# Performance work log

Measured on AMD Instinct MI355X. Metric: run time of the kernel, lower is better.

## Reference

```python
import jax, jax.numpy as jnp
import numpy as np

N = 100000
E = 3200000
IN_C = 500
HID = 256
OUT_C = 64
K = 10


def setup_inputs() -> dict:
    key = jax.random.key(0)
    k1, k2, k3, k4, k5 = jax.random.split(key, 5)
    node_feat = jax.random.normal(k1, (N, IN_C), dtype=jnp.float32)
    edge_index = jax.random.randint(k2, (2, E), 0, N, dtype=jnp.int64)
    # learned params (torch nn.Linear: y = x @ W.T + b)
    s1 = 1.0 / np.sqrt(IN_C)
    W1 = jax.random.uniform(k3, (HID, IN_C), jnp.float32, -s1, s1)
    b1 = jnp.zeros((HID,), jnp.float32)
    s2 = 1.0 / np.sqrt(HID)
    W2 = jax.random.uniform(k4, (OUT_C, HID), jnp.float32, -s2, s2)
    b2 = jnp.zeros((OUT_C,), jnp.float32)
    s3 = 1.0 / np.sqrt(OUT_C)
    proj_w = jax.random.uniform(k5, (OUT_C,), jnp.float32, -s3, s3)
    proj_b = jnp.zeros((), jnp.float32)
    return {"node_feat": node_feat, "edge_index": edge_index,
            "W1": W1, "b1": b1, "W2": W2, "b2": b2,
            "proj_w": proj_w, "proj_b": proj_b}


def reference(node_feat, edge_index, W1, b1, W2, b2, proj_w, proj_b):
    # MLP part (dropout p=0.0 / eval -> identity)
    x = jax.nn.relu(node_feat @ W1.T + b1)      # [N, HID]
    x = x @ W2.T + b2                            # [N, OUT_C]

    # gcn_norm with add_remaining_self_loops(fill=1):
    # existing self loops are dropped and replaced by unit-weight loops; with
    # all-ones edge_weight this equals zero-weighting self-loop edges and
    # appending N unit-weight self loops (static shapes, same math).
    row, col = edge_index[0], edge_index[1]
    loop = jnp.arange(N, dtype=edge_index.dtype)
    w = (row != col).astype(x.dtype)             # [E]
    full_row = jnp.concatenate([row, loop])      # [E+N]
    full_col = jnp.concatenate([col, loop])
    full_w = jnp.concatenate([w, jnp.ones((N,), x.dtype)])
    deg = jax.ops.segment_sum(full_w, full_col, num_segments=N)
    dinv = jnp.where(deg > 0, deg ** -0.5, 0.0).astype(x.dtype)
    norm = dinv[full_row] * full_w * dinv[full_col]  # [E+N]

    # K-hop propagation: gather -> scale -> scatter-add
    preds = [x]
    for _ in range(K):
        msg = norm[:, None] * x[full_row]        # [E+N, OUT_C]
        x = jax.ops.segment_sum(msg, full_col, num_segments=N)
        preds.append(x)
    pps = jnp.stack(preds, axis=1)               # [N, K+1, OUT_C]

    # sigmoid attention combine: proj = Linear(OUT_C, 1)
    score = jax.nn.sigmoid(jnp.einsum('nkc,c->nk', pps, proj_w) + proj_b)
    out = jnp.einsum('nk,nkc->nc', score, pps)   # [N, OUT_C]
    return out
```

## Files before the change

### kernel.cpp

```cpp
#include <hip/hip_runtime.h>
#include <math.h>

#define NN 100000
#define EE 3200000
#define INC 500
#define HIDN 256
#define OC 64
#define KHOP 10

typedef __attribute__((ext_vector_type(4))) float f4;
typedef __attribute__((ext_vector_type(4))) unsigned short us4;
typedef __attribute__((ext_vector_type(8))) unsigned short us8;

__device__ __forceinline__ float bf2f(unsigned short u) {
    return __uint_as_float(((unsigned int)u) << 16);
}
__device__ __forceinline__ unsigned short f2bf(float f) {
    unsigned int i = __float_as_uint(f);
    i += 0x7fffu + ((i >> 16) & 1u);
    return (unsigned short)(i >> 16);
}

__global__ __launch_bounds__(256) void gemm1_k(
    const float* __restrict__ feat, const float* __restrict__ W1,
    const float* __restrict__ b1, unsigned short* __restrict__ h)
{
    __shared__ float sA[16][64];
    __shared__ float sB[16][256];
    const int t  = threadIdx.x;
    const int m0 = blockIdx.x * 64;
    const int tx = t & 31;
    const int ty = t >> 5;
    float acc[8][8];
#pragma unroll
    for (int i = 0; i < 8; ++i)
#pragma unroll
        for (int j = 0; j < 8; ++j) acc[i][j] = 0.f;

    const int sm  = t >> 2;
    const int skq = (t & 3) * 4;

    for (int k0 = 0; k0 < INC; k0 += 16) {
        {
            int m = m0 + sm;
            f4 v = {0.f, 0.f, 0.f, 0.f};
            if (m < NN) {
                if (k0 + skq + 3 < INC) {
                    v = *reinterpret_cast<const f4*>(&feat[(size_t)m * INC + k0 + skq]);
                } else {
#pragma unroll
                    for (int i = 0; i < 4; ++i) {
                        int k = k0 + skq + i;
                        if (k < INC) v[i] = feat[(size_t)m * INC + k];
                    }
                }
            }
#pragma unroll
            for (int i = 0; i < 4; ++i) sA[skq + i][sm] = v[i];
        }
#pragma unroll
        for (int p = 0; p < 4; ++p) {
            int j = sm + p * 64;
            f4 v = {0.f, 0.f, 0.f, 0.f};
            if (k0 + skq + 3 < INC) {
                v = *reinterpret_cast<const f4*>(&W1[(size_t)j * INC + k0 + skq]);
            } else {
#pragma unroll
                for (int i = 0; i < 4; ++i) {
                    int k = k0 + skq + i;
                    if (k < INC) v[i] = W1[(size_t)j * INC + k];
                }
            }
#pragma unroll
            for (int i = 0; i < 4; ++i) sB[skq + i][j] = v[i];
        }
        __syncthreads();
#pragma unroll
        for (int k = 0; k < 16; ++k) {
            f4 a0 = *reinterpret_cast<const f4*>(&sA[k][ty * 8]);
            f4 a1 = *reinterpret_cast<const f4*>(&sA[k][ty * 8 + 4]);
            f4 c0 = *reinterpret_cast<const f4*>(&sB[k][tx * 4]);
            f4 c1 = *reinterpret_cast<const f4*>(&sB[k][128 + tx * 4]);
            float a[8] = {a0[0], a0[1], a0[2], a0[3], a1[0], a1[1], a1[2], a1[3]};
            float b[8] = {c0[0], c0[1], c0[2], c0[3], c1[0], c1[1], c1[2], c1[3]};
#pragma unroll
            for (int i = 0; i < 8; ++i)
#pragma unroll
                for (int j = 0; j < 8; ++j) acc[i][j] += a[i] * b[j];
        }
        __syncthreads();
    }
#pragma unroll
    for (int i = 0; i < 8; ++i) {
        int m = m0 + ty * 8 + i;
        if (m >= NN) continue;
        us4 o0, o1;
#pragma unroll
        for (int j = 0; j < 4; ++j) {
            float v0 = acc[i][j] + b1[tx * 4 + j];
            o0[j] = f2bf(v0 > 0.f ? v0 : 0.f);
            float v1 = acc[i][j + 4] + b1[128 + tx * 4 + j];
            o1[j] = f2bf(v1 > 0.f ? v1 : 0.f);
        }
        *reinterpret_cast<us4*>(&h[(size_t)m * HIDN + tx * 4]) = o0;
        *reinterpret_cast<us4*>(&h[(size_t)m * HIDN + 128 + tx * 4]) = o1;
    }
}

__global__ __launch_bounds__(256) void gemm2_k(
    const unsigned short* __restrict__ h, const float* __restrict__ W2,
    const float* __restrict__ b2, const float* __restrict__ pw,
    const float* __restrict__ pbp, float* __restrict__ out,
    unsigned short* __restrict__ xb)
{
    __shared__ unsigned short sA[32][64];
    __shared__ float sB[32][64];
    __shared__ float sX[64][65];
    const int t  = threadIdx.x;
    const int m0 = blockIdx.x * 64;
    const int tx = t & 15;
    const int ty = t >> 4;
    float acc[4][4];
#pragma unroll
    for (int i = 0; i < 4; ++i)
#pragma unroll
        for (int j = 0; j < 4; ++j) acc[i][j] = 0.f;

    const int am  = t >> 2;
    const int akq = (t & 3) * 8;

    for (int k0 = 0; k0 < HIDN; k0 += 32) {
        {
            int m = m0 + am;
            us8 v;
#pragma unroll
            for (int i = 0; i < 8; ++i) v[i] = 0;
            if (m < NN)
                v = *reinterpret_cast<const us8*>(&h[(size_t)m * HIDN + k0 + akq]);
#pragma unroll
            for (int i = 0; i < 8; ++i) sA[akq + i][am] = v[i];
        }
#pragma unroll
        for (int p = 0; p < 2; ++p) {
            int fid = t + p * 256;
            int c   = fid >> 3;
            int kq  = (fid & 7) * 4;
            f4 v = *reinterpret_cast<const f4*>(&W2[(size_t)c * HIDN + k0 + kq]);
#pragma unroll
            for (int i = 0; i < 4; ++i) sB[kq + i][c] = v[i];
        }
        __syncthreads();
#pragma unroll
        for (int k = 0; k < 32; ++k) {
            us4 av = *reinterpret_cast<const us4*>(&sA[k][ty * 4]);
            f4  bv = *reinterpret_cast<const f4*>(&sB[k][tx * 4]);
            float a[4] = {bf2f(av[0]), bf2f(av[1]), bf2f(av[2]), bf2f(av[3])};
#pragma unroll
            for (int i = 0; i < 4; ++i)
#pragma unroll
                for (int j = 0; j < 4; ++j) acc[i][j] += a[i] * bv[j];
        }
        __syncthreads();
    }
#pragma unroll
    for (int i = 0; i < 4; ++i)
#pragma unroll
        for (int j = 0; j < 4; ++j)
            sX[ty * 4 + i][tx * 4 + j] = acc[i][j] + b2[tx * 4 + j];
    __syncthreads();
    const int row  = t >> 2;
    const int part = t & 3;
    float v = 0.f;
#pragma unroll
    for (int i = 0; i < 16; ++i) {
        int c = part * 16 + i;
        v += sX[row][c] * pw[c];
    }
    v += __shfl_xor(v, 1);
    v += __shfl_xor(v, 2);
    float s = 1.f / (1.f + expf(-(v + pbp[0])));
    int m = m0 + row;
    if (m < NN) {
#pragma unroll
        for (int i = 0; i < 16; ++i) {
            int c = part * 16 + i;
            float val = sX[row][c];
            out[(size_t)m * OC + c] = s * val;
            xb[(size_t)m * OC + c]  = f2bf(val);
        }
    }
}

__global__ void deg_k(const int* __restrict__ ei, int* __restrict__ cnt) {
    int e = blockIdx.x * blockDim.x + threadIdx.x;
    if (e >= EE) return;
    int r = ei[e], c = ei[EE + e];
    if (r != c) atomicAdd(&cnt[c], 1);
}

__global__ __launch_bounds__(256) void scan1_k(const int* __restrict__ cnt,
                                               int* __restrict__ tmp,
                                               int* __restrict__ bsum) {
    __shared__ int sd[256];
    int t = threadIdx.x;
    int i = blockIdx.x * 256 + t;
    int v = (i < NN) ? cnt[i] : 0;
    int x = v;
    sd[t] = x;
    __syncthreads();
    for (int off = 1; off < 256; off <<= 1) {
        int y = (t >= off) ? sd[t - off] : 0;
        __syncthreads();
        x += y;
        sd[t] = x;
        __syncthreads();
    }
    if (i < NN) tmp[i] = x;
    if (t == 255) bsum[blockIdx.x] = x;
}

__global__ __launch_bounds__(512) void scan2_k(const int* __restrict__ bsum,
                                               int* __restrict__ boff, int nb) {
    __shared__ int sd[512];
    int t = threadIdx.x;
    int v = (t < nb) ? bsum[t] : 0;
    int x = v;
    sd[t] = x;
    __syncthreads();
    for (int off = 1; off < 512; off <<= 1) {
        int y = (t >= off) ? sd[t - off] : 0;
        __syncthreads();
        x += y;
        sd[t] = x;
        __syncthreads();
    }
    boff[t] = x - v;
}

__global__ __launch_bounds__(256) void scan3_k(const int* __restrict__ cnt,
                                               const int* __restrict__ tmp,
                                               const int* __restrict__ boff,
                                               int* __restrict__ rowptr) {
    int i = blockIdx.x * 256 + threadIdx.x;
    if (i < NN) {
        rowptr[i] = boff[blockIdx.x] + tmp[i] - cnt[i];
        if (i == NN - 1) rowptr[NN] = boff[blockIdx.x] + tmp[i];
    }
}

__global__ void dinv_k(const int* __restrict__ cnt, float* __restrict__ dinv) {
    int i = blockIdx.x * blockDim.x + threadIdx.x;
    if (i < NN) dinv[i] = rsqrtf((float)cnt[i] + 1.0f);
}

__global__ void fill_k(const int* __restrict__ ei, const int* __restrict__ rowptr,
                       int* __restrict__ fpos, const float* __restrict__ dinv,
                       int* __restrict__ csrc, float* __restrict__ cnrm) {
    int e = blockIdx.x * blockDim.x + threadIdx.x;
    if (e >= EE) return;
    int r = ei[e], c = ei[EE + e];
    if (r != c) {
        int p = rowptr[c] + atomicAdd(&fpos[c], 1);
        csrc[p] = r;
        cnrm[p] = dinv[r] * dinv[c];
    }
}

__global__ __launch_bounds__(256) void prop_k(
    const unsigned short* __restrict__ xin, unsigned short* __restrict__ xout,
    const int* __restrict__ rowptr, const int* __restrict__ csrc,
    const float* __restrict__ cnrm, const float* __restrict__ dinv,
    const float* __restrict__ pw, const float* __restrict__ pbp,
    float* __restrict__ out)
{
    int wid  = blockIdx.x * 4 + (threadIdx.x >> 6);
    int lane = threadIdx.x & 63;
    if (wid >= NN) return;
    float di = dinv[wid];
    float a0 = di * di * bf2f(xin[(size_t)wid * OC + lane]);
    float a1 = 0.f, a2 = 0.f, a3 = 0.f;
    int p0 = rowptr[wid], p1 = rowptr[wid + 1];
    for (int base = p0; base < p1; base += 64) {
        int n = p1 - base;
        if (n > 64) n = 64;
        int   sv = 0;
        float wv = 0.f;
        if (lane < n) {
            sv = csrc[base + lane];
            wv = cnrm[base + lane];
        }
        int j = 0;
        for (; j + 4 <= n; j += 4) {
            int   r0 = __shfl(sv, j    );
            int   r1 = __shfl(sv, j + 1);
            int   r2 = __shfl(sv, j + 2);
            int   r3 = __shfl(sv, j + 3);
            float w0 = __shfl(wv, j    );
            float w1 = __shfl(wv, j + 1);
            float w2 = __shfl(wv, j + 2);
            float w3 = __shfl(wv, j + 3);
            float x0 = bf2f(xin[(size_t)r0 * OC + lane]);
            float x1 = bf2f(xin[(size_t)r1 * OC + lane]);
            float x2 = bf2f(xin[(size_t)r2 * OC + lane]);
            float x3 = bf2f(xin[(size_t)r3 * OC + lane]);
            a0 += w0 * x0;
            a1 += w1 * x1;
            a2 += w2 * x2;
            a3 += w3 * x3;
        }
        for (; j < n; ++j) {
            int   r  = __shfl(sv, j);
            float wj = __shfl(wv, j);
            a0 += wj * bf2f(xin[(size_t)r * OC + lane]);
        }
    }
    float acc = (a0 + a1) + (a2 + a3);
    xout[(size_t)wid * OC + lane] = f2bf(acc);
    float v = acc * pw[lane];
#pragma unroll
    for (int off = 32; off > 0; off >>= 1) v += __shfl_xor(v, off);
    float s = 1.f / (1.f + expf(-(v + pbp[0])));
    out[(size_t)wid * OC + lane] += s * acc;
}

extern "C" void kernel_launch(void* const* d_in, const int* in_sizes, int n_in,
                              void* d_out, int out_size, void* d_ws, size_t ws_size,
                              hipStream_t stream)
{
    (void)in_sizes; (void)n_in; (void)out_size; (void)ws_size;
    const float* feat = (const float*)d_in[0];
    const int*   ei   = (const int*)d_in[1];
    const float* W1   = (const float*)d_in[2];
    const float* b1   = (const float*)d_in[3];
    const float* W2   = (const float*)d_in[4];
    const float* b2   = (const float*)d_in[5];
    const float* pw   = (const float*)d_in[6];
    const float* pbp  = (const float*)d_in[7];
    float* out = (float*)d_out;

    char* w = (char*)d_ws;
    auto carve = [&](size_t bytes) {
        char* p = w;
        w += (bytes + 255) & ~(size_t)255;
        return p;
    };
    unsigned short* h    = (unsigned short*)carve((size_t)NN * HIDN * 2);
    unsigned short* xb0  = (unsigned short*)carve((size_t)NN * OC * 2);
    unsigned short* xb1  = (unsigned short*)carve((size_t)NN * OC * 2);
    int*   csrc   = (int*)carve((size_t)EE * 4);
    float* cnrm   = (float*)carve((size_t)EE * 4);
    int*   cnt    = (int*)carve((size_t)NN * 4);
    int*   tmp    = (int*)carve((size_t)NN * 4);
    int*   bsum   = (int*)carve(4096);
    int*   boff   = (int*)carve(4096);
    int*   rowptr = (int*)carve((size_t)(NN + 1) * 4);
    int*   fpos   = (int*)carve((size_t)NN * 4);
    float* dinv   = (float*)carve((size_t)NN * 4);

    hipMemsetAsync(cnt, 0, (size_t)NN * 4, stream);
    hipMemsetAsync(fpos, 0, (size_t)NN * 4, stream);

    gemm1_k<<<1563, 256, 0, stream>>>(feat, W1, b1, h);
    deg_k<<<12500, 256, 0, stream>>>(ei, cnt);
    scan1_k<<<391, 256, 0, stream>>>(cnt, tmp, bsum);
    scan2_k<<<1, 512, 0, stream>>>(bsum, boff, 391);
    scan3_k<<<391, 256, 0, stream>>>(cnt, tmp, boff, rowptr);
    dinv_k<<<391, 256, 0, stream>>>(cnt, dinv);
    fill_k<<<12500, 256, 0, stream>>>(ei, rowptr, fpos, dinv, csrc, cnrm);
    gemm2_k<<<1563, 256, 0, stream>>>(h, W2, b2, pw, pbp, out, xb0);

    unsigned short* xi = xb0;
    unsigned short* xo = xb1;
    for (int k = 0; k < KHOP; ++k) {
        prop_k<<<25000, 256, 0, stream>>>(xi, xo, rowptr, csrc, cnrm, dinv, pw, pbp, out);
        unsigned short* t2 = xi; xi = xo; xo = t2;
    }
}
```

Measured before the change: 1.777 ms.

## Use bf16 MFMA for first GEMM, pack edge arrays, defer attention combine

The first GEMM moves from scalar FP32 FMA to bf16 MFMA 16x16x32 instructions. Operands are converted to bf16 when staged into padded shared memory, and K is zero-padded to 512. Edge source index and norm are packed into one int2 array so each propagation loop needs a single load. When the workspace is large enough, every hop's features are kept and one combine kernel computes the sigmoid-weighted sum, instead of a read-modify-write of the fp32 output after each hop. Converting the GEMM inputs to bf16 reduces precision.

```diff
diff --git a/kernel.cpp b/kernel.cpp
--- a/kernel.cpp
+++ b/kernel.cpp
@@ -7,10 +7,13 @@
 #define HIDN 256
 #define OC 64
 #define KHOP 10
+#define LDA 40
 
 typedef __attribute__((ext_vector_type(4))) float f4;
 typedef __attribute__((ext_vector_type(4))) unsigned short us4;
 typedef __attribute__((ext_vector_type(8))) unsigned short us8;
+typedef __attribute__((ext_vector_type(8))) short short8;
+typedef __attribute__((ext_vector_type(4))) float f32x4;
 
 __device__ __forceinline__ float bf2f(unsigned short u) {
     return __uint_as_float(((unsigned int)u) << 16);
@@ -20,90 +23,96 @@
     i += 0x7fffu + ((i >> 16) & 1u);
     return (unsigned short)(i >> 16);
 }
+__device__ __forceinline__ us8 pack8(f4 a, f4 b) {
+    us8 r;
+    r[0] = f2bf(a[0]); r[1] = f2bf(a[1]); r[2] = f2bf(a[2]); r[3] = f2bf(a[3]);
+    r[4] = f2bf(b[0]); r[5] = f2bf(b[1]); r[6] = f2bf(b[2]); r[7] = f2bf(b[3]);
+    return r;
+}
 
 __global__ __launch_bounds__(256) void gemm1_k(
     const float* __restrict__ feat, const float* __restrict__ W1,
     const float* __restrict__ b1, unsigned short* __restrict__ h)
 {
-    __shared__ float sA[16][64];
-    __shared__ float sB[16][256];
-    const int t  = threadIdx.x;
-    const int m0 = blockIdx.x * 64;
-    const int tx = t & 31;
-    const int ty = t >> 5;
-    float acc[8][8];
-#pragma unroll
-    for (int i = 0; i < 8; ++i)
-#pragma unroll
-        for (int j = 0; j < 8; ++j) acc[i][j] = 0.f;
-
-    const int sm  = t >> 2;
-    const int skq = (t & 3) * 4;
-
-    for (int k0 = 0; k0 < INC; k0 += 16) {
+    __shared__ unsigned short sA[64 * LDA];
+    __shared__ unsigned short sB[256 * LDA];
+
+    const int t    = threadIdx.x;
+    const int m0   = blockIdx.x * 64;
+    const int wc   = t >> 6;
+    const int lane = t & 63;
+    const int lg   = lane >> 4;
+    const int lm   = lane & 15;
+
+    f32x4 acc[4][4];
+#pragma unroll
+    for (int i = 0; i < 4; ++i)
+#pragma unroll
+        for (int j = 0; j < 4; ++j) acc[i][j] = (f32x4){0.f, 0.f, 0.f, 0.f};
+
+    const int arow = t >> 2;
+    const int akq  = (t & 3) * 8;
+
+    for (int k0 = 0; k0 < 512; k0 += 32) {
         {
-            int m = m0 + sm;
-            f4 v = {0.f, 0.f, 0.f, 0.f};
-            if (m < NN) {
-                if (k0 + skq + 3 < INC) {
-                    v = *reinterpret_cast<const f4*>(&feat[(size_t)m * INC + k0 + skq]);
-                } else {
-#pragma unroll
-                    for (int i = 0; i < 4; ++i) {
-                        int k = k0 + skq + i;
-                        if (k < INC) v[i] = feat[(size_t)m * INC + k];
-                    }
-                }
+            int gm = m0 + arow;
+            int kk = k0 + akq;
+            f4 va = {0.f, 0.f, 0.f, 0.f}, vb = {0.f, 0.f, 0.f, 0.f};
+            if (gm < NN) {
+                const float* p = &feat[(size_t)gm * INC + kk];
+                if (kk     < INC) va = *reinterpret_cast<const f4*>(p);
+                if (kk + 4 < INC) vb = *reinterpret_cast<const f4*>(p + 4);
             }
-#pragma unroll
-            for (int i = 0; i < 4; ++i) sA[skq + i][sm] = v[i];
-        }
-#pragma unroll
-        for (int p = 0; p < 4; ++p) {
-            int j = sm + p * 64;
-            f4 v = {0.f, 0.f, 0.f, 0.f};
-            if (k0 + skq + 3 < INC) {
-                v = *reinterpret_cast<const f4*>(&W1[(size_t)j * INC + k0 + skq]);
-            } else {
-#pragma unroll
-                for (int i = 0; i < 4; ++i) {
-                    int k = k0 + skq + i;
-                    if (k < INC) v[i] = W1[(size_t)j * INC + k];
-                }
+            *reinterpret_cast<us8*>(&sA[arow * LDA + akq]) = pack8(va, vb);
+        }
+#pragma unroll
+        for (int p = 0; p < 2; ++p) {
+            int fid = t + p * 256;
+            int row = fid >> 1;
+            int kq  = (fid & 1) * 16;
+            int kk  = k0 + kq;
+            const float* pp = &W1[(size_t)row * INC + kk];
+            f4 v0 = {0.f,0.f,0.f,0.f}, v1 = {0.f,0.f,0.f,0.f};
+            f4 v2 = {0.f,0.f,0.f,0.f}, v3 = {0.f,0.f,0.f,0.f};
+            if (kk      < INC) v0 = *reinterpret_cast<const f4*>(pp);
+            if (kk + 4  < INC) v1 = *reinterpret_cast<const f4*>(pp + 4);
+            if (kk + 8  < INC) v2 = *reinterpret_cast<const f4*>(pp + 8);
+            if (kk + 12 < INC) v3 = *reinterpret_cast<const f4*>(pp + 12);
+            *reinterpret_cast<us8*>(&sB[row * LDA + kq])     = pack8(v0, v1);
+            *reinterpret_cast<us8*>(&sB[row * LDA + kq + 8]) = pack8(v2, v3);
+        }
+        __syncthreads();
+        short8 aF[4], bF[4];
+#pragma unroll
+        for (int mi = 0; mi < 4; ++mi)
+            aF[mi] = *reinterpret_cast<const short8*>(&sA[(mi * 16 + lm) * LDA + lg * 8]);
+#pragma unroll
+        for (int ni = 0; ni < 4; ++ni)
+            bF[ni] = *reinterpret_cast<const short8*>(&sB[(wc * 64 + ni * 16 + lm) * LDA + lg * 8]);
+#pragma unroll
+        for (int mi = 0; mi < 4; ++mi)
+#pragma unroll
+            for (int ni = 0; ni < 4; ++ni)
+                acc[mi][ni] = __builtin_amdgcn_mfma_f32_16x16x32_bf16(
+                    aF[mi], bF[ni], acc[mi][ni], 0, 0, 0);
+        __syncthreads();
+    }
+    float bias[4];
+#pragma unroll
+    for (int ni = 0; ni < 4; ++ni) bias[ni] = b1[wc * 64 + ni * 16 + lm];
+#pragma unroll
+    for (int mi = 0; mi < 4; ++mi) {
+#pragma unroll
+        for (int r = 0; r < 4; ++r) {
+            int row = m0 + mi * 16 + lg * 4 + r;
+            if (row >= NN) continue;
+            size_t base = (size_t)row * HIDN + wc * 64;
+#pragma unroll
+            for (int ni = 0; ni < 4; ++ni) {
+                float v = acc[mi][ni][r] + bias[ni];
+                h[base + ni * 16 + lm] = f2bf(v > 0.f ? v : 0.f);
             }
-#pragma unroll
-            for (int i = 0; i < 4; ++i) sB[skq + i][j] = v[i];
-        }
-        __syncthreads();
-#pragma unroll
-        for (int k = 0; k < 16; ++k) {
-            f4 a0 = *reinterpret_cast<const f4*>(&sA[k][ty * 8]);
-            f4 a1 = *reinterpret_cast<const f4*>(&sA[k][ty * 8 + 4]);
-            f4 c0 = *reinterpret_cast<const f4*>(&sB[k][tx * 4]);
-            f4 c1 = *reinterpret_cast<const f4*>(&sB[k][128 + tx * 4]);
-            float a[8] = {a0[0], a0[1], a0[2], a0[3], a1[0], a1[1], a1[2], a1[3]};
-            float b[8] = {c0[0], c0[1], c0[2], c0[3], c1[0], c1[1], c1[2], c1[3]};
-#pragma unroll
-            for (int i = 0; i < 8; ++i)
-#pragma unroll
-                for (int j = 0; j < 8; ++j) acc[i][j] += a[i] * b[j];
-        }
-        __syncthreads();
-    }
-#pragma unroll
-    for (int i = 0; i < 8; ++i) {
-        int m = m0 + ty * 8 + i;
-        if (m >= NN) continue;
-        us4 o0, o1;
-#pragma unroll
-        for (int j = 0; j < 4; ++j) {
-            float v0 = acc[i][j] + b1[tx * 4 + j];
-            o0[j] = f2bf(v0 > 0.f ? v0 : 0.f);
-            float v1 = acc[i][j + 4] + b1[128 + tx * 4 + j];
-            o1[j] = f2bf(v1 > 0.f ? v1 : 0.f);
-        }
-        *reinterpret_cast<us4*>(&h[(size_t)m * HIDN + tx * 4]) = o0;
-        *reinterpret_cast<us4*>(&h[(size_t)m * HIDN + 128 + tx * 4]) = o1;
+        }
     }
 }
 
@@ -111,7 +120,7 @@
     const unsigned short* __restrict__ h, const float* __restrict__ W2,
     const float* __restrict__ b2, const float* __restrict__ pw,
     const float* __restrict__ pbp, float* __restrict__ out,
-    unsigned short* __restrict__ xb)
+    unsigned short* __restrict__ xb, int writeOut)
 {
     __shared__ unsigned short sA[32][64];
     __shared__ float sB[32][64];
@@ -185,8 +194,8 @@
         for (int i = 0; i < 16; ++i) {
             int c = part * 16 + i;
             float val = sX[row][c];
-            out[(size_t)m * OC + c] = s * val;
-            xb[(size_t)m * OC + c]  = f2bf(val);
+            if (writeOut) out[(size_t)m * OC + c] = s * val;
+            xb[(size_t)m * OC + c] = f2bf(val);
         }
     }
 }
@@ -255,23 +264,22 @@
 
 __global__ void fill_k(const int* __restrict__ ei, const int* __restrict__ rowptr,
                        int* __restrict__ fpos, const float* __restrict__ dinv,
-                       int* __restrict__ csrc, float* __restrict__ cnrm) {
+                       int2* __restrict__ epk) {
     int e = blockIdx.x * blockDim.x + threadIdx.x;
     if (e >= EE) return;
     int r = ei[e], c = ei[EE + e];
     if (r != c) {
         int p = rowptr[c] + atomicAdd(&fpos[c], 1);
-        csrc[p] = r;
-        cnrm[p] = dinv[r] * dinv[c];
-    }
-}
-
+        epk[p] = make_int2(r, __float_as_int(dinv[r] * dinv[c]));
+    }
+}
+
+template <int ACCUM>
 __global__ __launch_bounds__(256) void prop_k(
     const unsigned short* __restrict__ xin, unsigned short* __restrict__ xout,
-    const int* __restrict__ rowptr, const int* __restrict__ csrc,
-    const float* __restrict__ cnrm, const float* __restrict__ dinv,
-    const float* __restrict__ pw, const float* __restrict__ pbp,
-    float* __restrict__ out)
+    const int* __restrict__ rowptr, const int2* __restrict__ epk,
+    const float* __restrict__ dinv, const float* __restrict__ pw,
+    const float* __restrict__ pbp, float* __restrict__ out)
 {
     int wid  = blockIdx.x * 4 + (threadIdx.x >> 6);
     int lane = threadIdx.x & 63;
@@ -283,12 +291,10 @@
     for (int base = p0; base < p1; base += 64) {
         int n = p1 - base;
         if (n > 64) n = 64;
-        int   sv = 0;
-        float wv = 0.f;
-        if (lane < n) {
-            sv = csrc[base + lane];
-            wv = cnrm[base + lane];
-        }
+        int2 e = make_int2(0, 0);
+        if (lane < n) e = epk[base + lane];
+        int   sv = e.x;
+        float wv = __int_as_float(e.y);
         int j = 0;
         for (; j + 4 <= n; j += 4) {
             int   r0 = __shfl(sv, j    );
@@ -316,18 +322,42 @@
     }
     float acc = (a0 + a1) + (a2 + a3);
     xout[(size_t)wid * OC + lane] = f2bf(acc);
-    float v = acc * pw[lane];
-#pragma unroll
-    for (int off = 32; off > 0; off >>= 1) v += __shfl_xor(v, off);
-    float s = 1.f / (1.f + expf(-(v + pbp[0])));
-    out[(size_t)wid * OC + lane] += s * acc;
+    if (ACCUM) {
+        float v = acc * pw[lane];
+#pragma unroll
+        for (int off = 32; off > 0; off >>= 1) v += __shfl_xor(v, off);
+        float s = 1.f / (1.f + expf(-(v + pbp[0])));
+        out[(size_t)wid * OC + lane] += s * acc;
+    }
+}
+
+__global__ __launch_bounds__(256) void combine_k(
+    const unsigned short* __restrict__ xs, const float* __restrict__ pw,
+    const float* __restrict__ pbp, float* __restrict__ out)
+{
+    int wid  = blockIdx.x * 4 + (threadIdx.x >> 6);
+    int lane = threadIdx.x & 63;
+    if (wid >= NN) return;
+    float pwl = pw[lane];
+    float pb  = pbp[0];
+    float o   = 0.f;
+#pragma unroll
+    for (int k = 0; k <= KHOP; ++k) {
+        float x = bf2f(xs[(size_t)k * NN * OC + (size_t)wid * OC + lane]);
+        float v = x * pwl;
+#pragma unroll
+        for (int off = 32; off > 0; off >>= 1) v += __shfl_xor(v, off);
+        float s = 1.f / (1.f + expf(-(v + pb)));
+        o += s * x;
+    }
+    out[(size_t)wid * OC + lane] = o;
 }
 
 extern "C" void kernel_launch(void* const* d_in, const int* in_sizes, int n_in,
                               void* d_out, int out_size, void* d_ws, size_t ws_size,
                               hipStream_t stream)
 {
-    (void)in_sizes; (void)n_in; (void)out_size; (void)ws_size;
+    (void)in_sizes; (void)n_in; (void)out_size;
     const float* feat = (const float*)d_in[0];
     const int*   ei   = (const int*)d_in[1];
     const float* W1   = (const float*)d_in[2];
@@ -339,16 +369,16 @@
     float* out = (float*)d_out;
 
     char* w = (char*)d_ws;
+    size_t used = 0;
     auto carve = [&](size_t bytes) {
-        char* p = w;
-        w += (bytes + 255) & ~(size_t)255;
+        char* p = w + used;
+        used += (bytes + 255) & ~(size_t)255;
         return p;
     };
-    unsigned short* h    = (unsigned short*)carve((size_t)NN * HIDN * 2);
-    unsigned short* xb0  = (unsigned short*)carve((size_t)NN * OC * 2);
-    unsigned short* xb1  = (unsigned short*)carve((size_t)NN * OC * 2);
-    int*   csrc   = (int*)carve((size_t)EE * 4);
-    float* cnrm   = (float*)carve((size_t)EE * 4);
+    const size_t XSZ = (size_t)NN * OC * 2;
+
+    unsigned short* h      = (unsigned short*)carve((size_t)NN * HIDN * 2);
+    int2*  epk    = (int2*)carve((size_t)EE * 8);
     int*   cnt    = (int*)carve((size_t)NN * 4);
     int*   tmp    = (int*)carve((size_t)NN * 4);
     int*   bsum   = (int*)carve(4096);
@@ -357,6 +387,9 @@
     int*   fpos   = (int*)carve((size_t)NN * 4);
     float* dinv   = (float*)carve((size_t)NN * 4);
 
+    bool big = (ws_size - used) >= (size_t)(KHOP + 1) * XSZ;
+    unsigned short* xs = (unsigned short*)carve(big ? (KHOP + 1) * XSZ : 2 * XSZ);
+
     hipMemsetAsync(cnt, 0, (size_t)NN * 4, stream);
     hipMemsetAsync(fpos, 0, (size_t)NN * 4, stream);
 
@@ -366,13 +399,25 @@
     scan2_k<<<1, 512, 0, stream>>>(bsum, boff, 391);
     scan3_k<<<391, 256, 0, stream>>>(cnt, tmp, boff, rowptr);
     dinv_k<<<391, 256, 0, stream>>>(cnt, dinv);
-    fill_k<<<12500, 256, 0, stream>>>(ei, rowptr, fpos, dinv, csrc, cnrm);
-    gemm2_k<<<1563, 256, 0, stream>>>(h, W2, b2, pw, pbp, out, xb0);
-
-    unsigned short* xi = xb0;
-    unsigned short* xo = xb1;
-    for (int k = 0; k < KHOP; ++k) {
-        prop_k<<<25000, 256, 0, stream>>>(xi, xo, rowptr, csrc, cnrm, dinv, pw, pbp, out);
-        unsigned short* t2 = xi; xi = xo; xo = t2;
-    }
-}
+    fill_k<<<12500, 256, 0, stream>>>(ei, rowptr, fpos, dinv, epk);
+    gemm2_k<<<1563, 256, 0, stream>>>(h, W2, b2, pw, pbp, out,
+                                      xs , big ? 0 : 1);
+
+    if (big) {
+        for (int k = 0; k < KHOP; ++k) {
+            unsigned short* xi = xs + (size_t)k * NN * OC;
+            unsigned short* xo = xs + (size_t)(k + 1) * NN * OC;
+            prop_k<0><<<25000, 256, 0, stream>>>(xi, xo, rowptr, epk, dinv,
+                                                 pw, pbp, out);
+        }
+        combine_k<<<25000, 256, 0, stream>>>(xs, pw, pbp, out);
+    } else {
+        unsigned short* xi = xs;
+        unsigned short* xo = xs + NN * OC;
+        for (int k = 0; k < KHOP; ++k) {
+            prop_k<1><<<25000, 256, 0, stream>>>(xi, xo, rowptr, epk, dinv,
+                                                 pw, pbp, out);
+            unsigned short* t2 = xi; xi = xo; xo = t2;
+        }
+    }
+}
```

Result: faster. 1.597 ms (-10.1%).
